# Kernel optimization log

Measured on AMD Instinct MI355X. Metric: run time of the kernel, lower is better.

## Reference

```python
import jax, jax.numpy as jnp
import numpy as np


def _sq_dist(q, k):
    # pairwise squared L2 distance: [B,H,L,D] x [B,H,M,D] -> [B,H,L,M]
    q2 = jnp.sum(q * q, axis=-1)[..., :, None]
    k2 = jnp.sum(k * k, axis=-1)[..., None, :]
    qk = jnp.einsum('bhld,bhmd->bhlm', q, k)
    return q2 + k2 - 2.0 * qk


def setup_inputs() -> dict:
    key = jax.random.key(0)
    k1, k2, k3 = jax.random.split(key, 3)
    B, H, L, D = 2, 8, 2048, 64
    query = jax.random.normal(k1, (B, H, L, D), dtype=jnp.float32)
    key_t = jax.random.normal(k2, (B, H, L, D), dtype=jnp.float32)
    mask = jnp.ones((B, L), dtype=jnp.float32)
    # mu param: normal(0, 0.5) * [0,1][:,None,None] -> first component zeroed
    mu = (jax.random.normal(k3, (2, H, D), dtype=jnp.float32) * 0.5
          * jnp.array([0.0, 1.0], dtype=jnp.float32)[:, None, None])
    pi = jnp.array([0.5, 0.5], dtype=jnp.float32)
    return {'query': query, 'key': key_t, 'mask': mask, 'mu': mu, 'pi': pi}


def reference(query, key, mask, mu, pi):
    D = query.shape[-1]
    var = D ** 0.5  # self.var = head_dim ** 0.5
    neg = 1e6 * (1.0 - mask[:, None, None, :])  # [B,1,1,L]
    pic = jnp.clip(pi, 0.0, 1.0)
    qk1 = (-0.5 / var) * _sq_dist(query, key - mu[0][None, :, None, :]) - neg
    qk2 = (-0.5 / var) * _sq_dist(query, key - mu[1][None, :, None, :]) - neg
    attn = jnp.exp(qk1) * pic[0] + jnp.exp(qk2) * pic[1]
    return attn / jnp.sum(attn, axis=-1, keepdims=True)
```

## Files before the change

### kernel.cpp

```cpp
#include <hip/hip_runtime.h>
#include <math.h>

#define B_ 2
#define H_ 8
#define L_ 2048
#define D_ 64
#define BM 32
#define BN 128
#define NJ (L_ / BN)
#define L2E 1.4426950408889634f

typedef __attribute__((ext_vector_type(8))) short short8;
typedef __attribute__((ext_vector_type(4))) float f4;

typedef __attribute__((address_space(3))) void lds_void_t;
typedef const __attribute__((address_space(1))) void gbl_void_t;
#define GLL16(gp, lp) __builtin_amdgcn_global_load_lds( \
    (gbl_void_t*)(gp), (lds_void_t*)(lp), 16, 0, 0)

#define MFMA16(a, b, c) __builtin_amdgcn_mfma_f32_16x16x32_bf16(a, b, c, 0, 0, 0)

struct LdsT {
  short8 kth[BN * 8];
  short8 ktl[BN * 8];
  float  muv[2][D_];
  float  er0[BM], er1[BM];
  float  red[4][BM];
  float2 ckt[BN];
};

__device__ inline void split8(const float4& a0, const float4& a1,
                              short8& hi, short8& lo) {
  float xs[8] = {a0.x, a0.y, a0.z, a0.w, a1.x, a1.y, a1.z, a1.w};
#pragma unroll
  for (int e = 0; e < 8; ++e) {
    unsigned u  = __float_as_uint(xs[e]);
    unsigned hb = (u + 0x8000u) & 0xFFFF0000u;
    float    r  = xs[e] - __uint_as_float(hb);
    unsigned lb = (__float_as_uint(r) + 0x8000u) >> 16;
    hi[e] = (short)(hb >> 16);
    lo[e] = (short)lb;
  }
}

__global__ __launch_bounds__(256) void prep_kernel(
    const float* __restrict__ k, const float* __restrict__ mask,
    const float* __restrict__ mu, float2* __restrict__ ck,
    short8* __restrict__ wh, short8* __restrict__ wl)
{
  int bh = blockIdx.x >> 3;
  int c  = (blockIdx.x & 7) * 256 + threadIdx.x;
  int b  = bh >> 3, h = bh & 7;
  const float s = -0.0625f;
  const float* kp  = k  + ((size_t)bh * L_ + c) * D_;
  const float* mu0 = mu + (size_t)h * D_;
  const float* mu1 = mu + (size_t)(H_ * D_) + (size_t)h * D_;
  float x[D_];
#pragma unroll
  for (int d = 0; d < D_; d += 4)
    *reinterpret_cast<float4*>(&x[d]) = *reinterpret_cast<const float4*>(kp + d);
  float s0 = 0.f, s1 = 0.f;
#pragma unroll
  for (int d = 0; d < D_; ++d) {
    float a = x[d] - mu0[d]; s0 += a * a;
    float bb = x[d] - mu1[d]; s1 += bb * bb;
  }
  float neg = 1.0e6f * (1.0f - mask[(size_t)b * L_ + c]);
  ck[(size_t)bh * L_ + c] = make_float2(exp2f((s * s0 - neg) * L2E),
                                        exp2f((s * s1 - neg) * L2E));
#pragma unroll
  for (int gp = 0; gp < 8; ++gp) {
    int g = gp ^ (c & 7);
    short8 hi, lo;
    split8(*reinterpret_cast<const float4*>(&x[8 * g]),
           *reinterpret_cast<const float4*>(&x[8 * g + 4]), hi, lo);
    size_t idx = ((size_t)bh * L_ + c) * 8 + gp;
    wh[idx] = hi;
    wl[idx] = lo;
  }
}

template <bool USE_WS>
__global__ __launch_bounds__(256, 4) void mg_kernel(
    const float* __restrict__ q, const float* __restrict__ kk,
    const float* __restrict__ mask, const float* __restrict__ mu,
    const float* __restrict__ pi, const float2* __restrict__ ckw,
    const short8* __restrict__ wh, const short8* __restrict__ wl,
    float* __restrict__ out)
{
  extern __shared__ __align__(16) char smem_raw[];
  LdsT& S = *reinterpret_cast<LdsT*>(smem_raw);
  const int t = threadIdx.x;
  int bid = blockIdx.x;
  int vwg = (bid & 7) * 128 + (bid >> 3);
  int bh  = vwg >> 6;
  int rb  = vwg & 63;
  int b = bh >> 3, h = bh & 7;
  int row0 = rb * BM;

  const int w  = t >> 6;
  const int ln = t & 63;
  const int ci = ln & 15;
  const int kg = ln >> 4;
  const int x7 = ci & 7;

  const float s   = -0.0625f;
  const float DDC = 0.125f * L2E;

  const float*  maskb = mask + (size_t)b * L_;
  const float2* ckb   = ckw + (size_t)bh * L_;
  const float4* kb4   = (const float4*)(kk + (size_t)bh * L_ * D_);
  const short8* whb   = wh + (size_t)bh * (L_ * 8);
  const short8* wlb   = wl + (size_t)bh * (L_ * 8);

  if (t < 2 * D_)
    S.muv[t >> 6][t & 63] =
        mu[(size_t)(t >> 6) * (H_ * D_) + (size_t)h * D_ + (t & 63)];

  short8 ah[2][2], al[2][2];
#pragma unroll
  for (int rk = 0; rk < 2; ++rk) {
    const float* qrow = q + ((size_t)bh * L_ + row0 + rk * 16 + ci) * D_;
#pragma unroll
    for (int h2 = 0; h2 < 2; ++h2) {
      float4 a0 = *reinterpret_cast<const float4*>(qrow + 32 * h2 + kg * 8);
      float4 a1 = *reinterpret_cast<const float4*>(qrow + 32 * h2 + kg * 8 + 4);
      split8(a0, a1, ah[rk][h2], al[rk][h2]);
    }
  }
  __syncthreads();

  if (t < BM) {
    float pi0 = fminf(fmaxf(pi[0], 0.f), 1.f);
    float pi1 = fminf(fmaxf(pi[1], 0.f), 1.f);
    const float* qr = q + ((size_t)bh * L_ + row0 + t) * D_;
    float a0 = 0.f, a1 = 0.f, a2 = 0.f;
#pragma unroll
    for (int dq = 0; dq < 16; ++dq) {
      float4 qv = *reinterpret_cast<const float4*>(qr + 4 * dq);
      a0 += qv.x * qv.x + qv.y * qv.y + qv.z * qv.z + qv.w * qv.w;
      a1 += qv.x * S.muv[0][4*dq] + qv.y * S.muv[0][4*dq+1] +
            qv.z * S.muv[0][4*dq+2] + qv.w * S.muv[0][4*dq+3];
      a2 += qv.x * S.muv[1][4*dq] + qv.y * S.muv[1][4*dq+1] +
            qv.z * S.muv[1][4*dq+2] + qv.w * S.muv[1][4*dq+3];
    }
    S.er0[t] = pi0 * exp2f((s * a0 + 2.f * s * a1) * L2E);
    S.er1[t] = pi1 * exp2f((s * a0 + 2.f * s * a2) * L2E);
  }
  __syncthreads();

  float e0r[2][4], e1r[2][4];
#pragma unroll
  for (int rk = 0; rk < 2; ++rk)
#pragma unroll
    for (int reg = 0; reg < 4; ++reg) {
      e0r[rk][reg] = S.er0[rk * 16 + kg * 4 + reg];
      e1r[rk][reg] = S.er1[rk * 16 + kg * 4 + reg];
    }

  float rsum[2][4] = {{0.f, 0.f, 0.f, 0.f}, {0.f, 0.f, 0.f, 0.f}};
#pragma unroll 1
  for (int j = 0; j < NJ; ++j) {
    __syncthreads();
    float2 ec[2];
    if (USE_WS) {
#pragma unroll
      for (int i = 0; i < 4; ++i)
        GLL16(whb + (size_t)j * (BN * 8) + t + 256 * i, &S.kth[t + 256 * i]);
#pragma unroll
      for (int i = 0; i < 4; ++i)
        GLL16(wlb + (size_t)j * (BN * 8) + t + 256 * i, &S.ktl[t + 256 * i]);
#pragma unroll
      for (int n = 0; n < 2; ++n)
        ec[n] = ckb[j * BN + w * 32 + 16 * n + ci];
      __syncthreads();
    } else {
#pragma unroll
      for (int i = 0; i < 4; ++i) {
        int u = t + 256 * i;
        int col = u >> 3, gp = u & 7, g = gp ^ (col & 7);
        float4 x0 = kb4[(size_t)(j * BN + col) * 16 + 2 * g];
        float4 x1 = kb4[(size_t)(j * BN + col) * 16 + 2 * g + 1];
        short8 hi, lo;
        split8(x0, x1, hi, lo);
        S.kth[u] = hi;
        S.ktl[u] = lo;
      }
      if (t < BN) {
        const float* kc = kk + ((size_t)bh * L_ + j * BN + t) * D_;
        float s0 = 0.f, s1 = 0.f;
#pragma unroll
        for (int dq = 0; dq < 16; ++dq) {
          float4 kv = *reinterpret_cast<const float4*>(kc + 4 * dq);
          float a;
          a = kv.x - S.muv[0][4*dq];   s0 += a * a;
          a = kv.y - S.muv[0][4*dq+1]; s0 += a * a;
          a = kv.z - S.muv[0][4*dq+2]; s0 += a * a;
          a = kv.w - S.muv[0][4*dq+3]; s0 += a * a;
          a = kv.x - S.muv[1][4*dq];   s1 += a * a;
          a = kv.y - S.muv[1][4*dq+1]; s1 += a * a;
          a = kv.z - S.muv[1][4*dq+2]; s1 += a * a;
          a = kv.w - S.muv[1][4*dq+3]; s1 += a * a;
        }
        float neg = 1.0e6f * (1.0f - maskb[j * BN + t]);
        S.ckt[t] = make_float2(exp2f((s * s0 - neg) * L2E),
                               exp2f((s * s1 - neg) * L2E));
      }
      __syncthreads();
#pragma unroll
      for (int n = 0; n < 2; ++n) ec[n] = S.ckt[w * 32 + 16 * n + ci];
    }

#pragma unroll
    for (int n = 0; n < 2; ++n) {
      int base = (w * 32 + n * 16 + ci) * 8;
      short8 b0h = S.kth[base + (kg ^ x7)];
      short8 b1h = S.kth[base + ((4 + kg) ^ x7)];
      short8 b0l = S.ktl[base + (kg ^ x7)];
      short8 b1l = S.ktl[base + ((4 + kg) ^ x7)];
#pragma unroll
      for (int rk = 0; rk < 2; ++rk) {
        f4 acc = {0.f, 0.f, 0.f, 0.f};
        acc = MFMA16(ah[rk][0], b0h, acc);
        acc = MFMA16(ah[rk][1], b1h, acc);
        acc = MFMA16(ah[rk][0], b0l, acc);
        acc = MFMA16(ah[rk][1], b1l, acc);
        acc = MFMA16(al[rk][0], b0h, acc);
        acc = MFMA16(al[rk][1], b1h, acc);
#pragma unroll
        for (int reg = 0; reg < 4; ++reg) {
          float g2 = __builtin_amdgcn_exp2f(DDC * acc[reg]);
          float m  = fmaf(e0r[rk][reg], ec[n].x, e1r[rk][reg] * ec[n].y);
          rsum[rk][reg] = fmaf(g2, m, rsum[rk][reg]);
        }
      }
    }
  }

#pragma unroll
  for (int rk = 0; rk < 2; ++rk)
#pragma unroll
    for (int reg = 0; reg < 4; ++reg) {
      float v = rsum[rk][reg];
      v += __shfl_xor(v, 1, 64);
      v += __shfl_xor(v, 2, 64);
      v += __shfl_xor(v, 4, 64);
      v += __shfl_xor(v, 8, 64);
      if (ci == 0) S.red[w][rk * 16 + kg * 4 + reg] = v;
    }
  __syncthreads();
#pragma unroll
  for (int rk = 0; rk < 2; ++rk)
#pragma unroll
    for (int reg = 0; reg < 4; ++reg) {
      int r = rk * 16 + kg * 4 + reg;
      float inv = 1.0f / (S.red[0][r] + S.red[1][r] + S.red[2][r] + S.red[3][r]);
      e0r[rk][reg] *= inv;
      e1r[rk][reg] *= inv;
    }

  float* obr = out + ((size_t)bh * L_ + row0 + kg * 4) * L_ + w * 32 + ci;
#pragma unroll 1
  for (int jj = 0; jj < NJ; ++jj) {
    const int j = NJ - 1 - jj;
    float2 ec[2];
    if (jj != 0) {
      __syncthreads();
      if (USE_WS) {
#pragma unroll
        for (int i = 0; i < 4; ++i)
          GLL16(whb + (size_t)j * (BN * 8) + t + 256 * i, &S.kth[t + 256 * i]);
#pragma unroll
        for (int i = 0; i < 4; ++i)
          GLL16(wlb + (size_t)j * (BN * 8) + t + 256 * i, &S.ktl[t + 256 * i]);
#pragma unroll
        for (int n = 0; n < 2; ++n)
          ec[n] = ckb[j * BN + w * 32 + 16 * n + ci];
        __syncthreads();
      } else {
#pragma unroll
        for (int i = 0; i < 4; ++i) {
          int u = t + 256 * i;
          int col = u >> 3, gp = u & 7, g = gp ^ (col & 7);
          float4 x0 = kb4[(size_t)(j * BN + col) * 16 + 2 * g];
          float4 x1 = kb4[(size_t)(j * BN + col) * 16 + 2 * g + 1];
          short8 hi, lo;
          split8(x0, x1, hi, lo);
          S.kth[u] = hi;
          S.ktl[u] = lo;
        }
        if (t < BN) {
          const float* kc = kk + ((size_t)bh * L_ + j * BN + t) * D_;
          float s0 = 0.f, s1 = 0.f;
#pragma unroll
          for (int dq = 0; dq < 16; ++dq) {
            float4 kv = *reinterpret_cast<const float4*>(kc + 4 * dq);
            float a;
            a = kv.x - S.muv[0][4*dq];   s0 += a * a;
            a = kv.y - S.muv[0][4*dq+1]; s0 += a * a;
            a = kv.z - S.muv[0][4*dq+2]; s0 += a * a;
            a = kv.w - S.muv[0][4*dq+3]; s0 += a * a;
            a = kv.x - S.muv[1][4*dq];   s1 += a * a;
            a = kv.y - S.muv[1][4*dq+1]; s1 += a * a;
            a = kv.z - S.muv[1][4*dq+2]; s1 += a * a;
            a = kv.w - S.muv[1][4*dq+3]; s1 += a * a;
          }
          float neg = 1.0e6f * (1.0f - maskb[j * BN + t]);
          S.ckt[t] = make_float2(exp2f((s * s0 - neg) * L2E),
                                 exp2f((s * s1 - neg) * L2E));
        }
        __syncthreads();
#pragma unroll
        for (int n = 0; n < 2; ++n) ec[n] = S.ckt[w * 32 + 16 * n + ci];
      }
    } else {
      if (USE_WS) {
#pragma unroll
        for (int n = 0; n < 2; ++n)
          ec[n] = ckb[j * BN + w * 32 + 16 * n + ci];
      } else {
#pragma unroll
        for (int n = 0; n < 2; ++n) ec[n] = S.ckt[w * 32 + 16 * n + ci];
      }
    }

#pragma unroll
    for (int n = 0; n < 2; ++n) {
      int base = (w * 32 + n * 16 + ci) * 8;
      short8 b0h = S.kth[base + (kg ^ x7)];
      short8 b1h = S.kth[base + ((4 + kg) ^ x7)];
      short8 b0l = S.ktl[base + (kg ^ x7)];
      short8 b1l = S.ktl[base + ((4 + kg) ^ x7)];
#pragma unroll
      for (int rk = 0; rk < 2; ++rk) {
        f4 acc = {0.f, 0.f, 0.f, 0.f};
        acc = MFMA16(ah[rk][0], b0h, acc);
        acc = MFMA16(ah[rk][1], b1h, acc);
        acc = MFMA16(ah[rk][0], b0l, acc);
        acc = MFMA16(ah[rk][1], b1l, acc);
        acc = MFMA16(al[rk][0], b0h, acc);
        acc = MFMA16(al[rk][1], b1h, acc);
#pragma unroll
        for (int reg = 0; reg < 4; ++reg) {
          float g2 = __builtin_amdgcn_exp2f(DDC * acc[reg]);
          float m  = fmaf(e0r[rk][reg], ec[n].x, e1r[rk][reg] * ec[n].y);
          float p  = g2 * m;
          __builtin_nontemporal_store(
              p, obr + (size_t)(rk * 16 + reg) * L_ + (j * BN + n * 16));
        }
      }
    }
  }
}

extern "C" void kernel_launch(void* const* d_in, const int* in_sizes, int n_in,
                              void* d_out, int out_size, void* d_ws, size_t ws_size,
                              hipStream_t stream) {
  const float* q    = (const float*)d_in[0];
  const float* k    = (const float*)d_in[1];
  const float* mask = (const float*)d_in[2];
  const float* mu   = (const float*)d_in[3];
  const float* pi   = (const float*)d_in[4];
  float* out = (float*)d_out;

  const size_t smem     = sizeof(LdsT);
  const size_t ck_bytes = (size_t)B_ * H_ * L_ * sizeof(float2);
  const size_t wp_bytes = (size_t)B_ * H_ * L_ * D_ * sizeof(short);
  const bool use_ws = (ws_size >= ck_bytes + 2 * wp_bytes) && (d_ws != nullptr);

  if (use_ws) {
    float2* ck = (float2*)d_ws;
    short8* wh = (short8*)((char*)d_ws + ck_bytes);
    short8* wl = (short8*)((char*)d_ws + ck_bytes + wp_bytes);
    (void)hipFuncSetAttribute(reinterpret_cast<const void*>(&mg_kernel<true>),
                              hipFuncAttributeMaxDynamicSharedMemorySize, (int)smem);
    prep_kernel<<<dim3(B_ * H_ * 8), dim3(256), 0, stream>>>(k, mask, mu, ck, wh, wl);
    mg_kernel<true><<<dim3(B_ * H_ * (L_ / BM)), dim3(256), smem, stream>>>(
        q, k, mask, mu, pi, ck, wh, wl, out);
  } else {
    (void)hipFuncSetAttribute(reinterpret_cast<const void*>(&mg_kernel<false>),
                              hipFuncAttributeMaxDynamicSharedMemorySize, (int)smem);
    mg_kernel<false><<<dim3(B_ * H_ * (L_ / BM)), dim3(256), smem, stream>>>(
        q, k, mask, mu, pi, nullptr, nullptr, nullptr, out);
  }
}
```

Baseline: 122.7 us.

## Double row tile to 64 with 512-thread blocks sharing staged key tiles

Raises the row tile from 32 to 64 and the block size to 512 threads, with two row groups of four waves sharing each staged hi/lo bf16 key tile in LDS. This halves the number of key tile loads per output row in both passes. It also preloads the full per-column exp coefficient array into LDS once per block instead of reading it from global memory every tile, and folds the duplicated staging code into a lambda. The cost is fewer blocks (512 instead of 1024) and a lower occupancy hint, which leaves less parallelism for hiding the latency of the write-bound second pass.

```diff
diff --git a/kernel.cpp b/kernel.cpp
--- a/kernel.cpp
+++ b/kernel.cpp
@@ -5,9 +5,10 @@
 #define H_ 8
 #define L_ 2048
 #define D_ 64
-#define BM 32
+#define BM 64
 #define BN 128
 #define NJ (L_ / BN)
+#define NT 512
 #define L2E 1.4426950408889634f
 
 typedef __attribute__((ext_vector_type(8))) short short8;
@@ -23,10 +24,10 @@
 struct LdsT {
   short8 kth[BN * 8];
   short8 ktl[BN * 8];
+  float2 cka[L_];
   float  muv[2][D_];
   float  er0[BM], er1[BM];
   float  red[4][BM];
-  float2 ckt[BN];
 };
 
 __device__ inline void split8(const float4& a0, const float4& a1,
@@ -81,7 +82,7 @@
 }
 
 template <bool USE_WS>
-__global__ __launch_bounds__(256, 4) void mg_kernel(
+__global__ __launch_bounds__(NT, 2) void mg_kernel(
     const float* __restrict__ q, const float* __restrict__ kk,
     const float* __restrict__ mask, const float* __restrict__ mu,
     const float* __restrict__ pi, const float2* __restrict__ ckw,
@@ -92,9 +93,9 @@
   LdsT& S = *reinterpret_cast<LdsT*>(smem_raw);
   const int t = threadIdx.x;
   int bid = blockIdx.x;
-  int vwg = (bid & 7) * 128 + (bid >> 3);
-  int bh  = vwg >> 6;
-  int rb  = vwg & 63;
+  int vwg = (bid & 7) * 64 + (bid >> 3);
+  int bh  = vwg >> 5;
+  int rb  = vwg & 31;
   int b = bh >> 3, h = bh & 7;
   int row0 = rb * BM;
 
@@ -103,6 +104,8 @@
   const int ci = ln & 15;
   const int kg = ln >> 4;
   const int x7 = ci & 7;
+  const int wc = w & 3;
+  const int wr = (w >> 2) * 32;
 
   const float s   = -0.0625f;
   const float DDC = 0.125f * L2E;
@@ -117,10 +120,18 @@
     S.muv[t >> 6][t & 63] =
         mu[(size_t)(t >> 6) * (H_ * D_) + (size_t)h * D_ + (t & 63)];
 
+  if (USE_WS) {
+#pragma unroll
+    for (int i = 0; i < 4; ++i) {
+      int u = t + NT * i;
+      S.cka[u] = ckb[u];
+    }
+  }
+
   short8 ah[2][2], al[2][2];
 #pragma unroll
   for (int rk = 0; rk < 2; ++rk) {
-    const float* qrow = q + ((size_t)bh * L_ + row0 + rk * 16 + ci) * D_;
+    const float* qrow = q + ((size_t)bh * L_ + row0 + wr + rk * 16 + ci) * D_;
 #pragma unroll
     for (int h2 = 0; h2 < 2; ++h2) {
       float4 a0 = *reinterpret_cast<const float4*>(qrow + 32 * h2 + kg * 8);
@@ -154,30 +165,22 @@
   for (int rk = 0; rk < 2; ++rk)
 #pragma unroll
     for (int reg = 0; reg < 4; ++reg) {
-      e0r[rk][reg] = S.er0[rk * 16 + kg * 4 + reg];
-      e1r[rk][reg] = S.er1[rk * 16 + kg * 4 + reg];
-    }
-
-  float rsum[2][4] = {{0.f, 0.f, 0.f, 0.f}, {0.f, 0.f, 0.f, 0.f}};
-#pragma unroll 1
-  for (int j = 0; j < NJ; ++j) {
-    __syncthreads();
-    float2 ec[2];
+      e0r[rk][reg] = S.er0[wr + rk * 16 + kg * 4 + reg];
+      e1r[rk][reg] = S.er1[wr + rk * 16 + kg * 4 + reg];
+    }
+
+  auto STAGE = [&](int j) {
     if (USE_WS) {
 #pragma unroll
-      for (int i = 0; i < 4; ++i)
-        GLL16(whb + (size_t)j * (BN * 8) + t + 256 * i, &S.kth[t + 256 * i]);
-#pragma unroll
-      for (int i = 0; i < 4; ++i)
-        GLL16(wlb + (size_t)j * (BN * 8) + t + 256 * i, &S.ktl[t + 256 * i]);
-#pragma unroll
-      for (int n = 0; n < 2; ++n)
-        ec[n] = ckb[j * BN + w * 32 + 16 * n + ci];
-      __syncthreads();
+      for (int i = 0; i < 2; ++i)
+        GLL16(whb + (size_t)j * (BN * 8) + t + NT * i, &S.kth[t + NT * i]);
+#pragma unroll
+      for (int i = 0; i < 2; ++i)
+        GLL16(wlb + (size_t)j * (BN * 8) + t + NT * i, &S.ktl[t + NT * i]);
     } else {
 #pragma unroll
-      for (int i = 0; i < 4; ++i) {
-        int u = t + 256 * i;
+      for (int i = 0; i < 2; ++i) {
+        int u = t + NT * i;
         int col = u >> 3, gp = u & 7, g = gp ^ (col & 7);
         float4 x0 = kb4[(size_t)(j * BN + col) * 16 + 2 * g];
         float4 x1 = kb4[(size_t)(j * BN + col) * 16 + 2 * g + 1];
@@ -203,17 +206,25 @@
           a = kv.w - S.muv[1][4*dq+3]; s1 += a * a;
         }
         float neg = 1.0e6f * (1.0f - maskb[j * BN + t]);
-        S.ckt[t] = make_float2(exp2f((s * s0 - neg) * L2E),
-                               exp2f((s * s1 - neg) * L2E));
+        S.cka[j * BN + t] = make_float2(exp2f((s * s0 - neg) * L2E),
+                                        exp2f((s * s1 - neg) * L2E));
       }
-      __syncthreads();
-#pragma unroll
-      for (int n = 0; n < 2; ++n) ec[n] = S.ckt[w * 32 + 16 * n + ci];
-    }
-
+    }
+  };
+
+  float rsum[2][4] = {{0.f, 0.f, 0.f, 0.f}, {0.f, 0.f, 0.f, 0.f}};
+#pragma unroll 1
+  for (int j = 0; j < NJ; ++j) {
+    __syncthreads();
+    STAGE(j);
+    __syncthreads();
+    float2 ec[2];
+#pragma unroll
+    for (int n = 0; n < 2; ++n)
+      ec[n] = S.cka[j * BN + wc * 32 + 16 * n + ci];
 #pragma unroll
     for (int n = 0; n < 2; ++n) {
-      int base = (w * 32 + n * 16 + ci) * 8;
+      int base = (wc * 32 + n * 16 + ci) * 8;
       short8 b0h = S.kth[base + (kg ^ x7)];
       short8 b1h = S.kth[base + ((4 + kg) ^ x7)];
       short8 b0l = S.ktl[base + (kg ^ x7)];
@@ -246,87 +257,35 @@
       v += __shfl_xor(v, 2, 64);
       v += __shfl_xor(v, 4, 64);
       v += __shfl_xor(v, 8, 64);
-      if (ci == 0) S.red[w][rk * 16 + kg * 4 + reg] = v;
+      if (ci == 0) S.red[wc][wr + rk * 16 + kg * 4 + reg] = v;
     }
   __syncthreads();
 #pragma unroll
   for (int rk = 0; rk < 2; ++rk)
 #pragma unroll
     for (int reg = 0; reg < 4; ++reg) {
-      int r = rk * 16 + kg * 4 + reg;
+      int r = wr + rk * 16 + kg * 4 + reg;
       float inv = 1.0f / (S.red[0][r] + S.red[1][r] + S.red[2][r] + S.red[3][r]);
       e0r[rk][reg] *= inv;
       e1r[rk][reg] *= inv;
     }
 
-  float* obr = out + ((size_t)bh * L_ + row0 + kg * 4) * L_ + w * 32 + ci;
+  float* ob = out + ((size_t)bh * L_ + row0 + wr + kg * 4) * L_ + wc * 32 + ci;
 #pragma unroll 1
   for (int jj = 0; jj < NJ; ++jj) {
     const int j = NJ - 1 - jj;
-    float2 ec[2];
     if (jj != 0) {
       __syncthreads();
-      if (USE_WS) {
-#pragma unroll
-        for (int i = 0; i < 4; ++i)
-          GLL16(whb + (size_t)j * (BN * 8) + t + 256 * i, &S.kth[t + 256 * i]);
-#pragma unroll
-        for (int i = 0; i < 4; ++i)
-          GLL16(wlb + (size_t)j * (BN * 8) + t + 256 * i, &S.ktl[t + 256 * i]);
-#pragma unroll
-        for (int n = 0; n < 2; ++n)
-          ec[n] = ckb[j * BN + w * 32 + 16 * n + ci];
-        __syncthreads();
-      } else {
-#pragma unroll
-        for (int i = 0; i < 4; ++i) {
-          int u = t + 256 * i;
-          int col = u >> 3, gp = u & 7, g = gp ^ (col & 7);
-          float4 x0 = kb4[(size_t)(j * BN + col) * 16 + 2 * g];
-          float4 x1 = kb4[(size_t)(j * BN + col) * 16 + 2 * g + 1];
-          short8 hi, lo;
-          split8(x0, x1, hi, lo);
-          S.kth[u] = hi;
-          S.ktl[u] = lo;
-        }
-        if (t < BN) {
-          const float* kc = kk + ((size_t)bh * L_ + j * BN + t) * D_;
-          float s0 = 0.f, s1 = 0.f;
-#pragma unroll
-          for (int dq = 0; dq < 16; ++dq) {
-            float4 kv = *reinterpret_cast<const float4*>(kc + 4 * dq);
-            float a;
-            a = kv.x - S.muv[0][4*dq];   s0 += a * a;
-            a = kv.y - S.muv[0][4*dq+1]; s0 += a * a;
-            a = kv.z - S.muv[0][4*dq+2]; s0 += a * a;
-            a = kv.w - S.muv[0][4*dq+3]; s0 += a * a;
-            a = kv.x - S.muv[1][4*dq];   s1 += a * a;
-            a = kv.y - S.muv[1][4*dq+1]; s1 += a * a;
-            a = kv.z - S.muv[1][4*dq+2]; s1 += a * a;
-            a = kv.w - S.muv[1][4*dq+3]; s1 += a * a;
-          }
-          float neg = 1.0e6f * (1.0f - maskb[j * BN + t]);
-          S.ckt[t] = make_float2(exp2f((s * s0 - neg) * L2E),
-                                 exp2f((s * s1 - neg) * L2E));
-        }
-        __syncthreads();
-#pragma unroll
-        for (int n = 0; n < 2; ++n) ec[n] = S.ckt[w * 32 + 16 * n + ci];
-      }
-    } else {
-      if (USE_WS) {
-#pragma unroll
-        for (int n = 0; n < 2; ++n)
-          ec[n] = ckb[j * BN + w * 32 + 16 * n + ci];
-      } else {
-#pragma unroll
-        for (int n = 0; n < 2; ++n) ec[n] = S.ckt[w * 32 + 16 * n + ci];
-      }
-    }
-
+      STAGE(j);
+      __syncthreads();
+    }
+    float2 ec[2];
+#pragma unroll
+    for (int n = 0; n < 2; ++n)
+      ec[n] = S.cka[j * BN + wc * 32 + 16 * n + ci];
 #pragma unroll
     for (int n = 0; n < 2; ++n) {
-      int base = (w * 32 + n * 16 + ci) * 8;
+      int base = (wc * 32 + n * 16 + ci) * 8;
       short8 b0h = S.kth[base + (kg ^ x7)];
       short8 b1h = S.kth[base + ((4 + kg) ^ x7)];
       short8 b0l = S.ktl[base + (kg ^ x7)];
@@ -346,7 +305,7 @@
           float m  = fmaf(e0r[rk][reg], ec[n].x, e1r[rk][reg] * ec[n].y);
           float p  = g2 * m;
           __builtin_nontemporal_store(
-              p, obr + (size_t)(rk * 16 + reg) * L_ + (j * BN + n * 16));
+              p, ob + (size_t)(rk * 16 + reg) * L_ + (j * BN + n * 16));
         }
       }
     }
@@ -375,12 +334,12 @@
     (void)hipFuncSetAttribute(reinterpret_cast<const void*>(&mg_kernel<true>),
                               hipFuncAttributeMaxDynamicSharedMemorySize, (int)smem);
     prep_kernel<<<dim3(B_ * H_ * 8), dim3(256), 0, stream>>>(k, mask, mu, ck, wh, wl);
-    mg_kernel<true><<<dim3(B_ * H_ * (L_ / BM)), dim3(256), smem, stream>>>(
+    mg_kernel<true><<<dim3(B_ * H_ * (L_ / BM)), dim3(NT), smem, stream>>>(
         q, k, mask, mu, pi, ck, wh, wl, out);
   } else {
     (void)hipFuncSetAttribute(reinterpret_cast<const void*>(&mg_kernel<false>),
                               hipFuncAttributeMaxDynamicSharedMemorySize, (int)smem);
-    mg_kernel<false><<<dim3(B_ * H_ * (L_ / BM)), dim3(256), smem, stream>>>(
+    mg_kernel<false><<<dim3(B_ * H_ * (L_ / BM)), dim3(NT), smem, stream>>>(
         q, k, mask, mu, pi, nullptr, nullptr, nullptr, out);
   }
 }
```

Result: no change. 121.6 us (-0.8%).
